# Kernel tuning notes

Measured on AMD Instinct MI355X. Metric: run time of the kernel, lower is better.

The kernel has to match this reference:

```python
import jax, jax.numpy as jnp
import numpy as np

B, S, D = 2, 2048, 1024
H, DH = 16, 64  # n_heads, d_head; D == H*DH
OUTPUT_SCALE = 1.0
EPS = 1e-08

def setup_inputs() -> dict:
    key = jax.random.key(0)
    k1, k2, k3 = jax.random.split(key, 3)
    x = jax.random.normal(k1, (B, S, D), dtype=jnp.float32)
    # causal-style mask would also work; use all-True [B,S,S] bool mask (True = attend)
    mask = jnp.tril(jnp.ones((S, S), dtype=bool))[None].repeat(B, axis=0)
    Wqkv = jax.random.normal(k2, (D, 3 * D), dtype=jnp.float32) * (1.0 / np.sqrt(D))
    Wo = jax.random.normal(k3, (D, D), dtype=jnp.float32) * (1.0 / np.sqrt(D))
    tau = jnp.full((H, 1, 1), float(DH) ** 0.5, dtype=jnp.float32)  # learned per-head temperature
    return {"x": x, "mask": mask, "Wqkv": Wqkv, "Wo": Wo, "tau": tau}

def reference(x, mask, Wqkv, Wo, tau):
    b, s, d = x.shape
    qkv = x @ Wqkv                                   # [B,S,3D]
    q, k, v = jnp.split(qkv, 3, axis=-1)
    # [B,S,D] -> [B,H,S,DH]
    q = q.reshape(b, s, H, DH).transpose(0, 2, 1, 3)
    k = k.reshape(b, s, H, DH).transpose(0, 2, 1, 3)
    v = v.reshape(b, s, H, DH).transpose(0, 2, 1, 3)
    # L2 normalize Q and K along head dim
    q = q / (jnp.linalg.norm(q, axis=-1, keepdims=True) + EPS)
    k = k / (jnp.linalg.norm(k, axis=-1, keepdims=True) + EPS)
    q = q * tau                                       # per-head learned temperature [H,1,1]
    logits = jnp.einsum('bhqd,bhkd->bhqk', q, k) / jnp.sqrt(jnp.float32(DH))
    m = mask if mask.ndim == 4 else mask[:, None, :, :]
    logits = jnp.where(m, logits, jnp.finfo(logits.dtype).min)
    w = jax.nn.softmax(logits, axis=-1)
    attn = jnp.einsum('bhqk,bhkd->bhqd', w, v)        # [B,H,S,DH]
    attn = attn.transpose(0, 2, 1, 3).reshape(b, s, d)
    return (attn @ Wo) * OUTPUT_SCALE
```

## Files before the change

### kernel.cpp

```cpp
#include <hip/hip_runtime.h>
#include <math.h>

#define BATCH 2
#define SEQ 2048
#define DMODEL 1024
#define NHEAD 16
#define DHEAD 64
#define QKV_COLS (3 * DMODEL)
#define EPS 1e-8f
#define LOG2E 1.44269504f

typedef short bf16x8 __attribute__((ext_vector_type(8)));
typedef float f32x4 __attribute__((ext_vector_type(4)));

static __device__ __forceinline__ unsigned short f2bf(float x) {
  unsigned u = __float_as_uint(x);
  u += 0x7fffu + ((u >> 16) & 1u);
  return (unsigned short)(u >> 16);
}

static __device__ __forceinline__ unsigned pkbf(float lo, float hi) {
  const unsigned ul = __float_as_uint(lo) + 0x8000u;
  const unsigned uh = __float_as_uint(hi) + 0x8000u;
  return __builtin_amdgcn_perm(uh, ul, 0x07060302);
}

static __device__ __forceinline__ void async_ld16(const unsigned short* g,
                                                  unsigned short* l) {
  __builtin_amdgcn_global_load_lds(
      (const __attribute__((address_space(1))) void*)g,
      (__attribute__((address_space(3))) void*)(unsigned int)(unsigned long long)l,
      16, 0, 0);
}

__global__ __launch_bounds__(256) void convert_x_kernel(
    const float* __restrict__ x, unsigned short* __restrict__ xb) {
  const size_t i = ((size_t)blockIdx.x * 256 + threadIdx.x) * 4;
  const float4 a = *(const float4*)(x + i);
  ushort4 r;
  r.x = f2bf(a.x); r.y = f2bf(a.y); r.z = f2bf(a.z); r.w = f2bf(a.w);
  *(ushort4*)(xb + i) = r;
}

__global__ __launch_bounds__(256) void transpose_w2_kernel(
    const float* __restrict__ W0, unsigned short* __restrict__ Wt0,
    const float* __restrict__ W1, unsigned short* __restrict__ Wt1) {
  __shared__ float tile[32][33];
  const int bx = blockIdx.x;
  const float* W;
  unsigned short* Wt;
  int N, n0;
  if (bx < 96) { W = W0; Wt = Wt0; N = QKV_COLS; n0 = bx * 32; }
  else         { W = W1; Wt = Wt1; N = DMODEL;   n0 = (bx - 96) * 32; }
  const int K = DMODEL;
  const int k0 = blockIdx.y * 32;
  const int tx = threadIdx.x, ty = threadIdx.y;
#pragma unroll
  for (int i = 0; i < 4; ++i)
    tile[ty + i * 8][tx] = W[(size_t)(k0 + ty + i * 8) * N + n0 + tx];
  __syncthreads();
#pragma unroll
  for (int i = 0; i < 4; ++i)
    Wt[(size_t)(n0 + ty + i * 8) * K + k0 + tx] = f2bf(tile[tx][ty + i * 8]);
}

__global__ __launch_bounds__(256) void sgemm_bf16_kernel(
    const unsigned short* __restrict__ A, const unsigned short* __restrict__ Bt,
    float* __restrict__ C, int M, int N, int K) {
  __shared__ unsigned short As[2][128 * 32];
  __shared__ unsigned short Bs[2][128 * 32];

  const int t = threadIdx.x;
  const int w = t >> 6;
  const int lane = t & 63;
  const int quad = lane >> 4;
  const int lr = lane & 15;
  const int wr = w >> 1, wc = w & 1;
  const int m0 = blockIdx.y * 128;
  const int n0 = blockIdx.x * 128;

  const int srow = w * 32 + (lane >> 2);
  const int scol = (lane & 3) * 8;
  const unsigned short* ga = A + (size_t)(m0 + srow) * K + scol;
  const unsigned short* gb = Bt + (size_t)(n0 + srow) * K + scol;

  auto stage = [&](int k0, int bb) {
#pragma unroll
    for (int i = 0; i < 2; ++i) {
      async_ld16(ga + (size_t)(i * 16) * K + k0, &As[bb][(w * 32 + i * 16) * 32]);
      async_ld16(gb + (size_t)(i * 16) * K + k0, &Bs[bb][(w * 32 + i * 16) * 32]);
    }
  };

  f32x4 acc[4][4];
  const f32x4 zero4 = {0.f, 0.f, 0.f, 0.f};
#pragma unroll
  for (int i = 0; i < 4; ++i)
#pragma unroll
    for (int j = 0; j < 4; ++j) acc[i][j] = zero4;

  stage(0, 0);
  int bb = 0;
  for (int k0 = 0; k0 < K; k0 += 32, bb ^= 1) {
    __syncthreads();
    if (k0 + 32 < K) stage(k0 + 32, bb ^ 1);

    bf16x8 af[4], bfr[4];
#pragma unroll
    for (int i = 0; i < 4; ++i)
      af[i] = *(const bf16x8*)&As[bb][(wr * 64 + i * 16 + lr) * 32 + quad * 8];
#pragma unroll
    for (int j = 0; j < 4; ++j)
      bfr[j] = *(const bf16x8*)&Bs[bb][(wc * 64 + j * 16 + lr) * 32 + quad * 8];
#pragma unroll
    for (int i = 0; i < 4; ++i)
#pragma unroll
      for (int j = 0; j < 4; ++j)
        acc[i][j] = __builtin_amdgcn_mfma_f32_16x16x32_bf16(af[i], bfr[j], acc[i][j], 0, 0, 0);
  }

#pragma unroll
  for (int i = 0; i < 4; ++i)
#pragma unroll
    for (int r = 0; r < 4; ++r) {
      float* c = C + (size_t)(m0 + wr * 64 + i * 16 + quad * 4 + r) * N + n0 + wc * 64 + lr;
#pragma unroll
      for (int j = 0; j < 4; ++j) c[j * 16] = acc[i][j][r];
    }
}

__global__ __launch_bounds__(256) void qkv_gemm_norm_kernel(
    const unsigned short* __restrict__ A, const unsigned short* __restrict__ Bt,
    const float* __restrict__ tau,
    unsigned short* __restrict__ Qh, unsigned short* __restrict__ Kh,
    unsigned short* __restrict__ Vh) {
  __shared__ unsigned short As[2][128 * 32];
  __shared__ unsigned short Bs[2][128 * 32];

  const int K = DMODEL, N = QKV_COLS;
  const int t = threadIdx.x;
  const int w = t >> 6;
  const int lane = t & 63;
  const int quad = lane >> 4;
  const int lr = lane & 15;
  const int wr = w >> 1, wc = w & 1;
  const int m0 = blockIdx.y * 128;
  const int n0 = blockIdx.x * 128;

  const int srow = w * 32 + (lane >> 2);
  const int scol = (lane & 3) * 8;
  const unsigned short* ga = A + (size_t)(m0 + srow) * K + scol;
  const unsigned short* gb = Bt + (size_t)(n0 + srow) * K + scol;

  auto stage = [&](int k0, int bb) {
#pragma unroll
    for (int i = 0; i < 2; ++i) {
      async_ld16(ga + (size_t)(i * 16) * K + k0, &As[bb][(w * 32 + i * 16) * 32]);
      async_ld16(gb + (size_t)(i * 16) * K + k0, &Bs[bb][(w * 32 + i * 16) * 32]);
    }
  };

  f32x4 acc[4][4];
  const f32x4 zero4 = {0.f, 0.f, 0.f, 0.f};
#pragma unroll
  for (int i = 0; i < 4; ++i)
#pragma unroll
    for (int j = 0; j < 4; ++j) acc[i][j] = zero4;

  stage(0, 0);
  int bb = 0;
  for (int k0 = 0; k0 < K; k0 += 32, bb ^= 1) {
    __syncthreads();
    if (k0 + 32 < K) stage(k0 + 32, bb ^ 1);

    bf16x8 af[4], bfr[4];
#pragma unroll
    for (int i = 0; i < 4; ++i)
      af[i] = *(const bf16x8*)&As[bb][(wr * 64 + i * 16 + lr) * 32 + quad * 8];
#pragma unroll
    for (int j = 0; j < 4; ++j)
      bfr[j] = *(const bf16x8*)&Bs[bb][(wc * 64 + j * 16 + lr) * 32 + quad * 8];
#pragma unroll
    for (int i = 0; i < 4; ++i)
#pragma unroll
      for (int j = 0; j < 4; ++j)
        acc[i][j] = __builtin_amdgcn_mfma_f32_16x16x32_bf16(af[i], bfr[j], acc[i][j], 0, 0, 0);
  }

  const int col0 = n0 + wc * 64;
  const int which = col0 >> 10;
  const int h = (col0 & 1023) >> 6;
  const float tsc = tau[h] * 0.125f * LOG2E;
  unsigned short* dst = (which == 0) ? Qh : (which == 1) ? Kh : Vh;

#pragma unroll
  for (int i = 0; i < 4; ++i)
#pragma unroll
    for (int r = 0; r < 4; ++r) {
      const int s = m0 + wr * 64 + i * 16 + quad * 4 + r;
      unsigned short* ar =
          dst + (((size_t)((s >> 11) * NHEAD + h)) * SEQ + (s & 2047)) * DHEAD;
      float scale;
      if (which == 2) {
        scale = 1.0f;
      } else {
        float ss = 0.f;
#pragma unroll
        for (int j = 0; j < 4; ++j) ss += acc[i][j][r] * acc[i][j][r];
        ss += __shfl_xor(ss, 1, 16);
        ss += __shfl_xor(ss, 2, 16);
        ss += __shfl_xor(ss, 4, 16);
        ss += __shfl_xor(ss, 8, 16);
        scale = 1.0f / (sqrtf(ss) + EPS);
        if (which == 0) scale *= tsc;
      }
#pragma unroll
      for (int j = 0; j < 4; ++j) ar[j * 16 + lr] = f2bf(acc[i][j][r] * scale);
    }
}

__global__ __launch_bounds__(256) void vtrans_kernel(
    const unsigned short* __restrict__ Vh, unsigned short* __restrict__ Vt) {
  __shared__ unsigned short tile[64][72];
  const int bh = blockIdx.x;
  const int s0 = blockIdx.y * 64;
  const int t = threadIdx.x;
  const int sr = t >> 2;
  const int dc = (t & 3) * 16;
  const unsigned short* src = Vh + ((size_t)bh * SEQ + s0 + sr) * DHEAD + dc;
  *(bf16x8*)&tile[sr][dc]     = *(const bf16x8*)(src);
  *(bf16x8*)&tile[sr][dc + 8] = *(const bf16x8*)(src + 8);
  __syncthreads();
  const int dr = t >> 2;
  const int sc = (t & 3) * 16;
  unsigned short buf[16];
#pragma unroll
  for (int i = 0; i < 16; ++i) buf[i] = tile[sc + i][dr];
  unsigned short* dst = Vt + ((size_t)bh * DHEAD + dr) * SEQ + s0 + sc;
  *(bf16x8*)dst       = *(const bf16x8*)buf;
  *(bf16x8*)(dst + 8) = *(const bf16x8*)(buf + 8);
}

#define PLS 72

__global__ __launch_bounds__(256, 2) void attn_kernel(
    const unsigned short* __restrict__ Qh, const unsigned short* __restrict__ Kh,
    const unsigned short* __restrict__ Vt, unsigned short* __restrict__ attnb) {
  __shared__ unsigned short Ks[2][2][64 * 32];
  __shared__ unsigned short Vs[2][2][64 * 32];
  __shared__ unsigned short Pl[4][2][16 * PLS];

  const int idx = blockIdx.x;
  const int pair = idx >> 5;
  const int qblk = (idx < 256) ? (15 - pair) : (pair - 8);
  const int bh = idx & 31;
  const int b = bh >> 4;
  const int h = bh & 15;
  const int t = threadIdx.x;
  const int w = t >> 6;
  const int lane = t & 63;
  const int quad = lane >> 4;
  const int lr = lane & 15;
  const int q0 = qblk * 128;
  const int kend = q0 + 128;

  const unsigned short* Qp = Qh + (size_t)bh * SEQ * DHEAD;
  const unsigned short* Kp = Kh + (size_t)bh * SEQ * DHEAD;
  const unsigned short* Vp = Vt + (size_t)bh * DHEAD * SEQ;

  const int srow = lane >> 2;
  const int scol = (lane & 3) * 8;
  const int f0 = w * 4;

  auto stage = [&](int k0, int bb) {
#pragma unroll
    for (int i = 0; i < 4; ++i) {
      const int fi = f0 + i;
      if (fi < 8) {
        const int hh = fi >> 2, seg = fi & 3;
        async_ld16(Kp + (size_t)(k0 + seg * 16 + srow) * DHEAD + hh * 32 + scol,
                   &Ks[bb][hh][seg * 512]);
      } else {
        const int g = fi - 8;
        const int cc = g >> 2, seg = g & 3;
        async_ld16(Vp + (size_t)(seg * 16 + srow) * SEQ + k0 + cc * 32 + scol,
                   &Vs[bb][cc][seg * 512]);
      }
    }
  };

  const int qb0 = q0 + w * 16;
  const int qb1 = q0 + 64 + w * 16;

  bf16x8 aq[2][2];
#pragma unroll
  for (int qt = 0; qt < 2; ++qt) {
    const unsigned short* qr = Qp + (size_t)((qt ? qb1 : qb0) + lr) * DHEAD;
    aq[qt][0] = *(const bf16x8*)(qr + quad * 8);
    aq[qt][1] = *(const bf16x8*)(qr + 32 + quad * 8);
  }

  const f32x4 zero4 = {0.f, 0.f, 0.f, 0.f};
  f32x4 o[2][4];
#pragma unroll
  for (int qt = 0; qt < 2; ++qt)
#pragma unroll
    for (int nt = 0; nt < 4; ++nt) o[qt][nt] = zero4;
  float l0 = 0.f, l1 = 0.f;

#define SOFTMAX_P(cArr, Pq, lAcc, qbt)                                       \
  do {                                                                       \
    float ps = 0.f;                                                          \
    if (k0 + 63 > (qbt)) {                                                   \
      const int qrow = (qbt) + lr;                                           \
      _Pragma("unroll")                                                      \
      for (int kt = 0; kt < 4; ++kt) {                                       \
        float p[4];                                                          \
        _Pragma("unroll")                                                    \
        for (int r = 0; r < 4; ++r) {                                        \
          const int key = k0 + kt * 16 + quad * 4 + r;                       \
          p[r] = (key <= qrow) ? exp2f(cArr[kt][r]) : 0.f;                   \
          ps += p[r];                                                        \
        }                                                                    \
        const unsigned lo = pkbf(p[0], p[1]);                                \
        const unsigned hi = pkbf(p[2], p[3]);                                \
        *(unsigned long long*)&(Pq)[lr * PLS + kt * 16 + quad * 4] =         \
            ((unsigned long long)hi << 32) | lo;                             \
      }                                                                      \
    } else {                                                                 \
      _Pragma("unroll")                                                      \
      for (int kt = 0; kt < 4; ++kt) {                                       \
        float p[4];                                                          \
        _Pragma("unroll")                                                    \
        for (int r = 0; r < 4; ++r) {                                        \
          p[r] = exp2f(cArr[kt][r]);                                         \
          ps += p[r];                                                        \
        }                                                                    \
        const unsigned lo = pkbf(p[0], p[1]);                                \
        const unsigned hi = pkbf(p[2], p[3]);                                \
        *(unsigned long long*)&(Pq)[lr * PLS + kt * 16 + quad * 4] =         \
            ((unsigned long long)hi << 32) | lo;                             \
      }                                                                      \
    }                                                                        \
    lAcc += ps;                                                              \
  } while (0)

  stage(0, 0);
  int bb = 0;
  for (int k0 = 0; k0 < kend; k0 += 64, bb ^= 1) {
    __syncthreads();
    if (k0 + 64 < kend) stage(k0 + 64, bb ^ 1);

    const bool a0 = (k0 <= qb0 + 15);

    f32x4 c0[4], c1[4];
#pragma unroll
    for (int kt = 0; kt < 4; ++kt) {
      const bf16x8 kf0 = *(const bf16x8*)&Ks[bb][0][(kt * 16 + lr) * 32 + quad * 8];
      const bf16x8 kf1 = *(const bf16x8*)&Ks[bb][1][(kt * 16 + lr) * 32 + quad * 8];
      if (a0) {
        f32x4 tt = __builtin_amdgcn_mfma_f32_16x16x32_bf16(kf0, aq[0][0], zero4, 0, 0, 0);
        c0[kt] = __builtin_amdgcn_mfma_f32_16x16x32_bf16(kf1, aq[0][1], tt, 0, 0, 0);
      }
      f32x4 tt1 = __builtin_amdgcn_mfma_f32_16x16x32_bf16(kf0, aq[1][0], zero4, 0, 0, 0);
      c1[kt] = __builtin_amdgcn_mfma_f32_16x16x32_bf16(kf1, aq[1][1], tt1, 0, 0, 0);
    }

    if (a0) SOFTMAX_P(c0, Pl[w][0], l0, qb0);
    SOFTMAX_P(c1, Pl[w][1], l1, qb1);

    bf16x8 vb[2][4];
#pragma unroll
    for (int c2 = 0; c2 < 2; ++c2)
#pragma unroll
      for (int nt = 0; nt < 4; ++nt)
        vb[c2][nt] = *(const bf16x8*)&Vs[bb][c2][(nt * 16 + lr) * 32 + quad * 8];
#pragma unroll
    for (int c2 = 0; c2 < 2; ++c2) {
      if (a0) {
        const bf16x8 pa0 = *(const bf16x8*)&Pl[w][0][lr * PLS + c2 * 32 + quad * 8];
#pragma unroll
        for (int nt = 0; nt < 4; ++nt)
          o[0][nt] = __builtin_amdgcn_mfma_f32_16x16x32_bf16(pa0, vb[c2][nt], o[0][nt], 0, 0, 0);
      }
      const bf16x8 pa1 = *(const bf16x8*)&Pl[w][1][lr * PLS + c2 * 32 + quad * 8];
#pragma unroll
      for (int nt = 0; nt < 4; ++nt)
        o[1][nt] = __builtin_amdgcn_mfma_f32_16x16x32_bf16(pa1, vb[c2][nt], o[1][nt], 0, 0, 0);
    }
  }
#undef SOFTMAX_P

#pragma unroll
  for (int qt = 0; qt < 2; ++qt) {
    float lt = qt ? l1 : l0;
    lt += __shfl_xor(lt, 16, 64);
    lt += __shfl_xor(lt, 32, 64);
    const float inv = 1.0f / lt;
    const int qbt = qt ? qb1 : qb0;
#pragma unroll
    for (int r = 0; r < 4; ++r) {
      const float invr = __shfl(inv, quad * 4 + r, 16);
      unsigned short* ar =
          attnb + ((size_t)(b * SEQ + qbt + quad * 4 + r)) * DMODEL + h * DHEAD;
#pragma unroll
      for (int nt = 0; nt < 4; ++nt) ar[nt * 16 + lr] = f2bf(o[qt][nt][r] * invr);
    }
  }
}

extern "C" void kernel_launch(void* const* d_in, const int* in_sizes, int n_in,
                              void* d_out, int out_size, void* d_ws, size_t ws_size,
                              hipStream_t stream) {
  const float* x    = (const float*)d_in[0];
  const float* Wqkv = (const float*)d_in[2];
  const float* Wo   = (const float*)d_in[3];
  const float* tau  = (const float*)d_in[4];
  float* out = (float*)d_out;

  unsigned short* attnb = (unsigned short*)d_ws;
  unsigned short* Qh = attnb + (size_t)BATCH * SEQ * DMODEL;
  unsigned short* Kh = Qh + (size_t)BATCH * NHEAD * SEQ * DHEAD;
  unsigned short* Vh = Kh + (size_t)BATCH * NHEAD * SEQ * DHEAD;
  unsigned short* Xb = Vh + (size_t)BATCH * NHEAD * SEQ * DHEAD;
  unsigned short* Wqkv_t = Xb + (size_t)BATCH * SEQ * DMODEL;
  unsigned short* Wo_t = Wqkv_t + (size_t)DMODEL * QKV_COLS;
  unsigned short* Vt = Wo_t + (size_t)DMODEL * DMODEL;

  const int M = BATCH * SEQ;

  convert_x_kernel<<<(M * DMODEL) / (256 * 4), 256, 0, stream>>>(x, Xb);
  transpose_w2_kernel<<<dim3(128, 32), dim3(32, 8), 0, stream>>>(
      Wqkv, Wqkv_t, Wo, Wo_t);

  qkv_gemm_norm_kernel<<<dim3(QKV_COLS / 128, M / 128), 256, 0, stream>>>(
      Xb, Wqkv_t, tau, Qh, Kh, Vh);

  vtrans_kernel<<<dim3(BATCH * NHEAD, SEQ / 64), 256, 0, stream>>>(Vh, Vt);

  attn_kernel<<<dim3(BATCH * NHEAD * SEQ / 128), 256, 0, stream>>>(
      Qh, Kh, Vt, attnb);

  sgemm_bf16_kernel<<<dim3(DMODEL / 128, M / 128), 256, 0, stream>>>(
      attnb, Wo_t, out, M, DMODEL, DMODEL);
}
```

Baseline: 210.5 us.

## Pair complementary causal query blocks per workgroup with 8 waves sequentially

The attention kernel now launches 256 workgroups of 512 threads. Each workgroup processes two complementary 128-row query blocks (15-j and j) one after the other over a single concatenated key loop, so every workgroup does a balanced amount of causal work. Each of the 8 waves owns 16 query rows instead of 4 waves owning two 16-row tiles each, which halves per-wave accumulators and the per-thread K/V staging. The cost is that K/V tiles for the short block are reloaded rather than shared, and there is only one workgroup per CU, with no overlap between two resident blocks.

New measurement: 429.3 us. +103.9%, slower.

```diff
diff --git a/kernel.cpp b/kernel.cpp
--- a/kernel.cpp
+++ b/kernel.cpp
@@ -243,17 +243,17 @@
 
 #define PLS 72
 
-__global__ __launch_bounds__(256, 2) void attn_kernel(
+__global__ __launch_bounds__(512, 1) void attn_kernel(
     const unsigned short* __restrict__ Qh, const unsigned short* __restrict__ Kh,
     const unsigned short* __restrict__ Vt, unsigned short* __restrict__ attnb) {
   __shared__ unsigned short Ks[2][2][64 * 32];
   __shared__ unsigned short Vs[2][2][64 * 32];
-  __shared__ unsigned short Pl[4][2][16 * PLS];
+  __shared__ unsigned short Pl[8][16 * PLS];
 
   const int idx = blockIdx.x;
-  const int pair = idx >> 5;
-  const int qblk = (idx < 256) ? (15 - pair) : (pair - 8);
   const int bh = idx & 31;
+  const int j = idx >> 5;
+  const int qA = 15 - j, qB = j;
   const int b = bh >> 4;
   const int h = bh & 15;
   const int t = threadIdx.x;
@@ -261,20 +261,19 @@
   const int lane = t & 63;
   const int quad = lane >> 4;
   const int lr = lane & 15;
-  const int q0 = qblk * 128;
-  const int kend = q0 + 128;
 
   const unsigned short* Qp = Qh + (size_t)bh * SEQ * DHEAD;
   const unsigned short* Kp = Kh + (size_t)bh * SEQ * DHEAD;
   const unsigned short* Vp = Vt + (size_t)bh * DHEAD * SEQ;
+  unsigned short* Pw = &Pl[w][0];
 
   const int srow = lane >> 2;
   const int scol = (lane & 3) * 8;
-  const int f0 = w * 4;
+  const int f0 = w * 2;
 
   auto stage = [&](int k0, int bb) {
 #pragma unroll
-    for (int i = 0; i < 4; ++i) {
+    for (int i = 0; i < 2; ++i) {
       const int fi = f0 + i;
       if (fi < 8) {
         const int hh = fi >> 2, seg = fi & 3;
@@ -289,124 +288,114 @@
     }
   };
 
-  const int qb0 = q0 + w * 16;
-  const int qb1 = q0 + 64 + w * 16;
-
   bf16x8 aq[2][2];
-#pragma unroll
-  for (int qt = 0; qt < 2; ++qt) {
-    const unsigned short* qr = Qp + (size_t)((qt ? qb1 : qb0) + lr) * DHEAD;
-    aq[qt][0] = *(const bf16x8*)(qr + quad * 8);
-    aq[qt][1] = *(const bf16x8*)(qr + 32 + quad * 8);
+  {
+    const unsigned short* qrA = Qp + (size_t)(qA * 128 + w * 16 + lr) * DHEAD;
+    const unsigned short* qrB = Qp + (size_t)(qB * 128 + w * 16 + lr) * DHEAD;
+    aq[0][0] = *(const bf16x8*)(qrA + quad * 8);
+    aq[0][1] = *(const bf16x8*)(qrA + 32 + quad * 8);
+    aq[1][0] = *(const bf16x8*)(qrB + quad * 8);
+    aq[1][1] = *(const bf16x8*)(qrB + 32 + quad * 8);
   }
 
   const f32x4 zero4 = {0.f, 0.f, 0.f, 0.f};
-  f32x4 o[2][4];
-#pragma unroll
-  for (int qt = 0; qt < 2; ++qt)
-#pragma unroll
-    for (int nt = 0; nt < 4; ++nt) o[qt][nt] = zero4;
-  float l0 = 0.f, l1 = 0.f;
-
-#define SOFTMAX_P(cArr, Pq, lAcc, qbt)                                       \
-  do {                                                                       \
-    float ps = 0.f;                                                          \
-    if (k0 + 63 > (qbt)) {                                                   \
-      const int qrow = (qbt) + lr;                                           \
-      _Pragma("unroll")                                                      \
-      for (int kt = 0; kt < 4; ++kt) {                                       \
-        float p[4];                                                          \
-        _Pragma("unroll")                                                    \
-        for (int r = 0; r < 4; ++r) {                                        \
-          const int key = k0 + kt * 16 + quad * 4 + r;                       \
-          p[r] = (key <= qrow) ? exp2f(cArr[kt][r]) : 0.f;                   \
-          ps += p[r];                                                        \
-        }                                                                    \
-        const unsigned lo = pkbf(p[0], p[1]);                                \
-        const unsigned hi = pkbf(p[2], p[3]);                                \
-        *(unsigned long long*)&(Pq)[lr * PLS + kt * 16 + quad * 4] =         \
-            ((unsigned long long)hi << 32) | lo;                             \
-      }                                                                      \
-    } else {                                                                 \
-      _Pragma("unroll")                                                      \
-      for (int kt = 0; kt < 4; ++kt) {                                       \
-        float p[4];                                                          \
-        _Pragma("unroll")                                                    \
-        for (int r = 0; r < 4; ++r) {                                        \
-          p[r] = exp2f(cArr[kt][r]);                                         \
-          ps += p[r];                                                        \
-        }                                                                    \
-        const unsigned lo = pkbf(p[0], p[1]);                                \
-        const unsigned hi = pkbf(p[2], p[3]);                                \
-        *(unsigned long long*)&(Pq)[lr * PLS + kt * 16 + quad * 4] =         \
-            ((unsigned long long)hi << 32) | lo;                             \
-      }                                                                      \
-    }                                                                        \
-    lAcc += ps;                                                              \
-  } while (0)
-
-  stage(0, 0);
-  int bb = 0;
-  for (int k0 = 0; k0 < kend; k0 += 64, bb ^= 1) {
-    __syncthreads();
-    if (k0 + 64 < kend) stage(k0 + 64, bb ^ 1);
-
-    const bool a0 = (k0 <= qb0 + 15);
-
-    f32x4 c0[4], c1[4];
-#pragma unroll
-    for (int kt = 0; kt < 4; ++kt) {
-      const bf16x8 kf0 = *(const bf16x8*)&Ks[bb][0][(kt * 16 + lr) * 32 + quad * 8];
-      const bf16x8 kf1 = *(const bf16x8*)&Ks[bb][1][(kt * 16 + lr) * 32 + quad * 8];
-      if (a0) {
-        f32x4 tt = __builtin_amdgcn_mfma_f32_16x16x32_bf16(kf0, aq[0][0], zero4, 0, 0, 0);
-        c0[kt] = __builtin_amdgcn_mfma_f32_16x16x32_bf16(kf1, aq[0][1], tt, 0, 0, 0);
-      }
-      f32x4 tt1 = __builtin_amdgcn_mfma_f32_16x16x32_bf16(kf0, aq[1][0], zero4, 0, 0, 0);
-      c1[kt] = __builtin_amdgcn_mfma_f32_16x16x32_bf16(kf1, aq[1][1], tt1, 0, 0, 0);
-    }
-
-    if (a0) SOFTMAX_P(c0, Pl[w][0], l0, qb0);
-    SOFTMAX_P(c1, Pl[w][1], l1, qb1);
-
-    bf16x8 vb[2][4];
-#pragma unroll
-    for (int c2 = 0; c2 < 2; ++c2)
-#pragma unroll
-      for (int nt = 0; nt < 4; ++nt)
-        vb[c2][nt] = *(const bf16x8*)&Vs[bb][c2][(nt * 16 + lr) * 32 + quad * 8];
-#pragma unroll
-    for (int c2 = 0; c2 < 2; ++c2) {
-      if (a0) {
-        const bf16x8 pa0 = *(const bf16x8*)&Pl[w][0][lr * PLS + c2 * 32 + quad * 8];
-#pragma unroll
-        for (int nt = 0; nt < 4; ++nt)
-          o[0][nt] = __builtin_amdgcn_mfma_f32_16x16x32_bf16(pa0, vb[c2][nt], o[0][nt], 0, 0, 0);
-      }
-      const bf16x8 pa1 = *(const bf16x8*)&Pl[w][1][lr * PLS + c2 * 32 + quad * 8];
-#pragma unroll
-      for (int nt = 0; nt < 4; ++nt)
-        o[1][nt] = __builtin_amdgcn_mfma_f32_16x16x32_bf16(pa1, vb[c2][nt], o[1][nt], 0, 0, 0);
-    }
-  }
-#undef SOFTMAX_P
-
-#pragma unroll
-  for (int qt = 0; qt < 2; ++qt) {
-    float lt = qt ? l1 : l0;
+  f32x4 o[4];
+  o[0] = o[1] = o[2] = o[3] = zero4;
+  float l_ = 0.f;
+
+  auto epilogue = [&](int qbt) {
+    float lt = l_;
     lt += __shfl_xor(lt, 16, 64);
     lt += __shfl_xor(lt, 32, 64);
     const float inv = 1.0f / lt;
-    const int qbt = qt ? qb1 : qb0;
 #pragma unroll
     for (int r = 0; r < 4; ++r) {
       const float invr = __shfl(inv, quad * 4 + r, 16);
       unsigned short* ar =
           attnb + ((size_t)(b * SEQ + qbt + quad * 4 + r)) * DMODEL + h * DHEAD;
 #pragma unroll
-      for (int nt = 0; nt < 4; ++nt) ar[nt * 16 + lr] = f2bf(o[qt][nt][r] * invr);
+      for (int nt = 0; nt < 4; ++nt) ar[nt * 16 + lr] = f2bf(o[nt][r] * invr);
+    }
+  };
+
+  const int sA = 2 * (qA + 1);
+  const int total = sA + 2 * (qB + 1);
+
+  stage(0, 0);
+  int bb = 0;
+  int ph = 0;
+  int q0 = qA * 128;
+  for (int s = 0; s < total; ++s, bb ^= 1) {
+    const int k0 = (s < sA ? s : s - sA) * 64;
+    __syncthreads();
+    const int ns = s + 1;
+    if (ns < total) stage((ns < sA ? ns : ns - sA) * 64, bb ^ 1);
+
+    const int qb = q0 + w * 16;
+    if (k0 <= qb + 15) {
+      f32x4 c[4];
+#pragma unroll
+      for (int kt = 0; kt < 4; ++kt) {
+        const bf16x8 kf0 = *(const bf16x8*)&Ks[bb][0][(kt * 16 + lr) * 32 + quad * 8];
+        const bf16x8 kf1 = *(const bf16x8*)&Ks[bb][1][(kt * 16 + lr) * 32 + quad * 8];
+        f32x4 tt = __builtin_amdgcn_mfma_f32_16x16x32_bf16(kf0, aq[ph][0], zero4, 0, 0, 0);
+        c[kt] = __builtin_amdgcn_mfma_f32_16x16x32_bf16(kf1, aq[ph][1], tt, 0, 0, 0);
+      }
+
+      float ps = 0.f;
+      if (k0 + 63 > qb) {
+        const int qrow = qb + lr;
+#pragma unroll
+        for (int kt = 0; kt < 4; ++kt) {
+          float p[4];
+#pragma unroll
+          for (int r = 0; r < 4; ++r) {
+            const int key = k0 + kt * 16 + quad * 4 + r;
+            p[r] = (key <= qrow) ? exp2f(c[kt][r]) : 0.f;
+            ps += p[r];
+          }
+          const unsigned lo = pkbf(p[0], p[1]);
+          const unsigned hi = pkbf(p[2], p[3]);
+          *(unsigned long long*)&Pw[lr * PLS + kt * 16 + quad * 4] =
+              ((unsigned long long)hi << 32) | lo;
+        }
+      } else {
+#pragma unroll
+        for (int kt = 0; kt < 4; ++kt) {
+          float p[4];
+#pragma unroll
+          for (int r = 0; r < 4; ++r) {
+            p[r] = exp2f(c[kt][r]);
+            ps += p[r];
+          }
+          const unsigned lo = pkbf(p[0], p[1]);
+          const unsigned hi = pkbf(p[2], p[3]);
+          *(unsigned long long*)&Pw[lr * PLS + kt * 16 + quad * 4] =
+              ((unsigned long long)hi << 32) | lo;
+        }
+      }
+      l_ += ps;
+
+#pragma unroll
+      for (int c2 = 0; c2 < 2; ++c2) {
+        const bf16x8 pa = *(const bf16x8*)&Pw[lr * PLS + c2 * 32 + quad * 8];
+#pragma unroll
+        for (int nt = 0; nt < 4; ++nt) {
+          const bf16x8 vb = *(const bf16x8*)&Vs[bb][c2][(nt * 16 + lr) * 32 + quad * 8];
+          o[nt] = __builtin_amdgcn_mfma_f32_16x16x32_bf16(pa, vb, o[nt], 0, 0, 0);
+        }
+      }
+    }
+
+    if (s == sA - 1) {
+      epilogue(qA * 128 + w * 16);
+      o[0] = o[1] = o[2] = o[3] = zero4;
+      l_ = 0.f;
+      ph = 1;
+      q0 = qB * 128;
     }
   }
+  epilogue(qB * 128 + w * 16);
 }
 
 extern "C" void kernel_launch(void* const* d_in, const int* in_sizes, int n_in,
@@ -438,8 +427,7 @@
 
   vtrans_kernel<<<dim3(BATCH * NHEAD, SEQ / 64), 256, 0, stream>>>(Vh, Vt);
 
-  attn_kernel<<<dim3(BATCH * NHEAD * SEQ / 128), 256, 0, stream>>>(
-      Qh, Kh, Vt, attnb);
+  attn_kernel<<<dim3(256), 512, 0, stream>>>(Qh, Kh, Vt, attnb);
 
   sgemm_bf16_kernel<<<dim3(DMODEL / 128, M / 128), 256, 0, stream>>>(
       attnb, Wo_t, out, M, DMODEL, DMODEL);
```
